# Performance work log

Measured on AMD Instinct MI355X. Metric: run time of the kernel, lower is better.

The kernel has to match this reference:

```python
import jax, jax.numpy as jnp
import numpy as np

EPS = 1e-5  # BatchNorm eps (torch default); BN is in training mode with gamma=1, beta=0 (init values)


def bn(x, axes):
    m = jnp.mean(x, axis=axes, keepdims=True)
    v = jnp.var(x, axis=axes, keepdims=True)
    return (x - m) * jax.lax.rsqrt(v + EPS)


def knn_idx(xyz, k):
    # brute-force squared-distance matrix [B,N,N], k smallest
    d = jnp.sum((xyz[:, :, None, :] - xyz[:, None, :, :]) ** 2, axis=-1)
    _, idx = jax.lax.top_k(-d, k)
    return idx  # [B,N,k]


def gather(x, idx):
    # x: [B,N,C], idx: [B,N,k] -> [B,N,k,C]
    return jax.vmap(lambda a, i: a[i])(x, idx)


def lse(xyz, features, idx, w):
    nbr_xyz = gather(xyz, idx)                       # [B,N,k,3]
    rel = nbr_xyz - xyz[:, :, None, :]
    dist = jnp.sqrt(jnp.maximum(jnp.sum(rel ** 2, -1, keepdims=True), 1e-12))
    nbr_f = gather(features, idx)                    # [B,N,k,C]
    enc = jnp.concatenate([rel, dist, nbr_f], -1)    # [B,N,k,C+4]
    return jax.nn.relu(bn(jnp.einsum('bnkc,oc->bnko', enc, w), (0, 1, 2)))


def att_pool(x, sw1, sw2, sb2, mw):
    # x: [B,N,k,C]
    h = jax.nn.relu(bn(jnp.einsum('bnkc,oc->bnko', x, sw1), (0, 1, 2)))
    scores = jax.nn.softmax(jnp.einsum('bnkc,oc->bnko', h, sw2) + sb2, axis=2)  # softmax over k
    feat = jnp.sum(x * scores, axis=2)               # [B,N,C]
    return jax.nn.relu(bn(jnp.einsum('bnc,oc->bno', feat, mw), (0, 1)))


def drb(x, w1, w2):
    # in_channels == out_channels -> identity shortcut
    h = jax.nn.relu(bn(jnp.einsum('bnc,oc->bno', x, w1), (0, 1)))
    h = bn(jnp.einsum('bnc,oc->bno', h, w2), (0, 1))
    return jax.nn.relu(h + x)


def setup_inputs() -> dict:
    key = jax.random.key(0)
    B, N, C, K, OUT = 4, 8192, 32, 16, 128
    H = OUT // 2  # 64
    ks = jax.random.split(key, 16)
    s = 0.05
    return {
        'xyz': jax.random.normal(ks[0], (B, N, 3), jnp.float32),
        'features': jax.random.normal(ks[1], (B, N, C), jnp.float32),
        'w_lse1': jax.random.normal(ks[2], (H, C + 4), jnp.float32) * s,
        'w_lse2': jax.random.normal(ks[3], (H, C + 4), jnp.float32) * s,
        'ap1_sw1': jax.random.normal(ks[4], (H, H), jnp.float32) * s,
        'ap1_sw2': jax.random.normal(ks[5], (1, H), jnp.float32) * s,
        'ap1_sb2': jax.random.normal(ks[6], (1,), jnp.float32) * s,
        'ap1_mw': jax.random.normal(ks[7], (H, H), jnp.float32) * s,
        'ap2_sw1': jax.random.normal(ks[8], (H, H), jnp.float32) * s,
        'ap2_sw2': jax.random.normal(ks[9], (1, H), jnp.float32) * s,
        'ap2_sb2': jax.random.normal(ks[10], (1,), jnp.float32) * s,
        'ap2_mw': jax.random.normal(ks[11], (H, H), jnp.float32) * s,
        'drb_w1': jax.random.normal(ks[12], (OUT, OUT), jnp.float32) * s,
        'drb_w2': jax.random.normal(ks[13], (OUT, OUT), jnp.float32) * s,
    }


def reference(xyz, features, w_lse1, w_lse2, ap1_sw1, ap1_sw2, ap1_sb2, ap1_mw,
              ap2_sw1, ap2_sw2, ap2_sb2, ap2_mw, drb_w1, drb_w2):
    K = 16
    idx = knn_idx(xyz, K)  # original calls knn twice on same xyz -> identical indices
    f1 = att_pool(lse(xyz, features, idx, w_lse1), ap1_sw1, ap1_sw2, ap1_sb2, ap1_mw)
    f2 = att_pool(lse(xyz, features, idx, w_lse2), ap2_sw1, ap2_sw2, ap2_sb2, ap2_mw)
    agg = jnp.concatenate([f1, f2], axis=-1)  # [B,N,128]
    return drb(agg, drb_w1, drb_w2)           # [B,N,128]
```

## Files before the change

### kernel.cpp

```cpp
#include <hip/hip_runtime.h>
#include <hip/hip_bf16.h>
#include <hip/hip_fp16.h>
#include <float.h>
#include <math.h>

#define DEVFN __device__ __forceinline__

DEVFN void wavefence() { __builtin_amdgcn_wave_barrier(); }

using half8 = __attribute__((ext_vector_type(8))) _Float16;
using f32x4 = __attribute__((ext_vector_type(4))) float;

namespace {
constexpr int Bq = 4, Nq = 8192, Cq = 32, Kq = 16;
constexpr int PTS = Bq * Nq;
constexpr int CH = 16;
constexpr int CAND = Nq / CH;
constexpr double ROWS = 524288.0;

constexpr int DS_Y = 0, DS_Z = 256, DS_G = 512, DS_H1 = 768, DS_H2 = 1024;

constexpr size_t OFF_KD   = 0;
constexpr size_t OFF_KJ   = (size_t)32 << 20;
constexpr size_t OFF_X0   = 0;
constexpr size_t OFF_X1   = (size_t)64 << 20;
constexpr size_t OFF_ENC  = (size_t)128 << 20;
constexpr size_t OFF_H1   = 0;
constexpr size_t OFF_H2   = (size_t)16 << 20;
constexpr size_t OFF_GRAW = (size_t)192 << 20;
constexpr size_t OFF_AGG  = (size_t)208 << 20;
constexpr size_t OFF_IDX  = (size_t)224 << 20;
constexpr size_t OFF_DST  = (size_t)226 << 20;
constexpr size_t OFF_MST  = ((size_t)226 << 20) + 10240;
constexpr size_t OFF_BNP  = ((size_t)226 << 20) + 16384;
constexpr size_t WS_NEED  = ((size_t)226 << 20) + 32768;
constexpr size_t FB_GRAW  = (size_t)64 << 20;
constexpr size_t FB_AGG   = (size_t)80 << 20;
constexpr size_t FB_H1    = (size_t)96 << 20;
constexpr size_t FB_H2    = (size_t)112 << 20;
constexpr size_t FB_IDX   = (size_t)128 << 20;
constexpr size_t FB_DST   = (size_t)130 << 20;
constexpr size_t FB_MST   = ((size_t)130 << 20) + 10240;
constexpr size_t FB_BNP   = ((size_t)130 << 20) + 16384;
}

DEVFN void ce_asc(float& a, float& b) {
  const float lo = fminf(a, b), hi = fmaxf(a, b);
  a = lo; b = hi;
}

DEVFN void topk16_update(float* __restrict__ L, float* __restrict__ d) {
#pragma unroll
  for (int k = 2; k <= 16; k <<= 1) {
#pragma unroll
    for (int j = k >> 1; j > 0; j >>= 1) {
#pragma unroll
      for (int i = 0; i < 16; ++i) {
        const int l = i ^ j;
        if (l > i) {
          if ((i & k) == 0) {
            const float lo = fminf(d[i], d[l]), hi = fmaxf(d[i], d[l]);
            d[i] = lo; d[l] = hi;
          } else {
            const float lo = fminf(d[i], d[l]), hi = fmaxf(d[i], d[l]);
            d[i] = hi; d[l] = lo;
          }
        }
      }
    }
  }
#pragma unroll
  for (int i = 0; i < 16; ++i) L[i] = fminf(L[i], d[15 - i]);
#pragma unroll
  for (int j = 8; j > 0; j >>= 1) {
#pragma unroll
    for (int i = 0; i < 16; ++i) {
      const int l = i ^ j;
      if (l > i) ce_asc(L[i], L[l]);
    }
  }
}

DEVFN float distf(const float4 c, const float qx, const float qy, const float qz) {
  const float dx = qx - c.x, dy = qy - c.y, dz = qz - c.z;
  return __fadd_rn(__fadd_rn(__fmul_rn(dx, dx), __fmul_rn(dy, dy)), __fmul_rn(dz, dz));
}

__global__ __launch_bounds__(256, 4) void knn_chunk_kernel(const float* __restrict__ xyz,
                                                           float* __restrict__ pd,
                                                           int* __restrict__ pj) {
  const int b = blockIdx.z;
  const int ch = blockIdx.y;
  const int n = blockIdx.x * 256 + threadIdx.x;
  __shared__ __align__(16) float4 tile[CAND];
  const float* xb = xyz + (size_t)b * Nq * 3;
  for (int t = threadIdx.x; t < CAND; t += 256) {
    const int j = ch * CAND + t;
    tile[t] = make_float4(xb[j * 3], xb[j * 3 + 1], xb[j * 3 + 2], 0.f);
  }
  __syncthreads();
  const float qx = xb[n * 3], qy = xb[n * 3 + 1], qz = xb[n * 3 + 2];
  float L[16];
#pragma unroll
  for (int i = 0; i < 16; ++i) L[i] = FLT_MAX;
  for (int t = 0; t < CAND; t += 16) {
    float d[16];
#pragma unroll
    for (int u = 0; u < 16; ++u) d[u] = distf(tile[t + u], qx, qy, qz);
// ... 110 lines not shown
    for (int q = 0; q < 4; ++q) {
      const __half2 xv = u.h[q];
      const __half2 wv = wh2[r * 4 + q];
      if (q & 1) {
        a2 += __low2float(xv) * __low2float(wv);
        a3 += __high2float(xv) * __high2float(wv);
      } else {
        a0 += __low2float(xv) * __low2float(wv);
        a1 += __high2float(xv) * __high2float(wv);
      }
    }
  }
  return (a0 + a1) + (a2 + a3);
}

DEVFN float dot64x(const __half* __restrict__ xr, const __half2* __restrict__ sh2) {
  float a0 = 0.f, a1 = 0.f, a2 = 0.f, a3 = 0.f;
#pragma unroll
  for (int r = 0; r < 8; ++r) {
    union { float4 f; __half2 h[4]; } u;
    u.f = *(const float4*)(xr + r * 8);
#pragma unroll
    for (int q = 0; q < 4; ++q) {
      const __half2 xv = u.h[q];
      const __half2 wv = sh2[r * 4 + q];
      if (q & 1) {
        a2 += __low2float(xv) * __low2float(wv);
        a3 += __high2float(xv) * __high2float(wv);
      } else {
        a0 += __low2float(xv) * __low2float(wv);
        a1 += __high2float(xv) * __high2float(wv);
      }
    }
  }
  return (a0 + a1) + (a2 + a3);
}

DEVFN void load_w40(const float* __restrict__ Wrow, __half2* wh2) {
#pragma unroll
  for (int c = 0; c < 16; ++c)
    wh2[c] = __floats2half2_rn(Wrow[4 + 2 * c], Wrow[5 + 2 * c]);
  wh2[16] = __floats2half2_rn(Wrow[0], Wrow[1]);
  wh2[17] = __floats2half2_rn(Wrow[2], Wrow[3]);
  wh2[18] = __floats2half2_rn(0.f, 0.f);
  wh2[19] = wh2[18];
}

DEVFN void load_b1(const float* __restrict__ W, int lane, half8* b1) {
  const int o16 = lane & 15, q = lane >> 4;
#pragma unroll
  for (int t = 0; t < 4; ++t) {
    const int o = t * 16 + o16;
#pragma unroll
    for (int ks = 0; ks < 2; ++ks) {
      half8 v;
#pragma unroll
      for (int j = 0; j < 8; ++j) {
        const int s = ks * 32 + q * 8 + j;
        float wv = 0.f;
        if (s < 36) { const int orig = (s < 32) ? (s + 4) : (s - 32); wv = W[o * 36 + orig]; }
        v[j] = (_Float16)wv;
      }
      b1[t * 2 + ks] = v;
    }
  }
}

DEVFN void load_b2(const float* __restrict__ S1, int lane, half8* b2) {
  const int o16 = lane & 15, q = lane >> 4;
#pragma unroll
  for (int t = 0; t < 4; ++t) {
    const int o = t * 16 + o16;
#pragma unroll
    for (int ks = 0; ks < 2; ++ks) {
      half8 v;
#pragma unroll
      for (int j = 0; j < 8; ++j) {
        const int c = ks * 32 + q * 8 + j;
        v[j] = (_Float16)S1[o * 64 + c];
      }
      b2[t * 2 + ks] = v;
    }
  }
}

#define GATHER_PROLOGUE                                                      \
  int p = wid;                                                               \
  int jc = issue_idx(idx, p, lane);                                          \
  PF cur = issue_feat(features, xyz, p, jc, lane & 3);                       \
  float3 qc = issue_query(xyz, p);                                           \
  int pn0 = p + nw; if (pn0 >= PTS) pn0 = p;                                 \
  int jn = issue_idx(idx, pn0, lane);                                        \
  float3 qn = issue_query(xyz, pn0);                                         \
  for (; p < PTS; p += nw) {                                                 \
    int pn = p + nw; if (pn >= PTS) pn = p;                                  \
    int pn2 = pn + nw; if (pn2 >= PTS) pn2 = pn;                             \
    PF nxt = issue_feat(features, xyz, pn, jn, lane & 3);                    \
    const int jn2 = issue_idx(idx, pn2, lane);                               \
    const float3 q2 = issue_query(xyz, pn2);                                 \
    commit_enc(enc, lane, cur, qc.x, qc.y, qc.z);                            \
    wavefence();

#define GATHER_EPILOGUE                                                      \
    wavefence();                                                             \
    cur = nxt; qc = qn; qn = q2; jn = jn2;                                   \
  }

__global__ __launch_bounds__(256)
void encM2_kernel(const float* __restrict__ xyz,
                  const float* __restrict__ features,
                  const int* __restrict__ idx,
                  const float* __restrict__ wl1,
                  const float* __restrict__ wl2,
                  double* __restrict__ dstat,
                  __half* __restrict__ encb) {
  __shared__ __align__(16) __half encS[4][16 * 40];
  const int lane = threadIdx.x & 63, wv = threadIdx.x >> 6;
  __half* enc = encS[wv];
  zero_enc_pad(enc, lane);
  wavefence();
  half8 b1a[8], b1b[8];
  load_b1(wl1, lane, b1a);
  load_b1(wl2, lane, b1b);
  const int r16 = lane & 15, q4 = lane >> 4;
  float ya1[4] = {0.f, 0.f, 0.f, 0.f}, ya2[4] = {0.f, 0.f, 0.f, 0.f};
  float yb1[4] = {0.f, 0.f, 0.f, 0.f}, yb2[4] = {0.f, 0.f, 0.f, 0.f};
  const int wid = blockIdx.x * 4 + wv, nw = gridDim.x * 4;
  GATHER_PROLOGUE
#pragma unroll
    for (int it = 0; it < 2; ++it) {
      const int c = it * 64 + lane;
      if (c < 80) {
        const float4 v = *(const float4*)((const char*)enc + c * 16);
        *(float4*)((char*)encb + (size_t)p * 1280 + c * 16) = v;
      }
    }
    const __half* er = enc + r16 * 40;
    const half8 a0 = *(const half8*)(er + q4 * 8);
    half8 a1;
#pragma unroll
    for (int j = 0; j < 8; ++j) a1[j] = (_Float16)0.f;
    if (q4 == 0) a1 = *(const half8*)(er + 32);
#pragma unroll
    for (int t = 0; t < 4; ++t) {
      f32x4 acc = {0.f, 0.f, 0.f, 0.f};
      acc = __builtin_amdgcn_mfma_f32_16x16x32_f16(a0, b1a[t * 2], acc, 0, 0, 0);
      acc = __builtin_amdgcn_mfma_f32_16x16x32_f16(a1, b1a[t * 2 + 1], acc, 0, 0, 0);
#pragma unroll
      for (int rr = 0; rr < 4; ++rr) { const float yv = acc[rr]; ya1[t] += yv; ya2[t] += yv * yv; }
      f32x4 acc2 = {0.f, 0.f, 0.f, 0.f};
      acc2 = __builtin_amdgcn_mfma_f32_16x16x32_f16(a0, b1b[t * 2], acc2, 0, 0, 0);
      acc2 = __builtin_amdgcn_mfma_f32_16x16x32_f16(a1, b1b[t * 2 + 1], acc2, 0, 0, 0);
#pragma unroll
      for (int rr = 0; rr < 4; ++rr) { const float yv = acc2[rr]; yb1[t] += yv; yb2[t] += yv * yv; }
    }
  GATHER_EPILOGUE
#pragma unroll
  for (int t = 0; t < 4; ++t) {
    ya1[t] += __shfl_xor(ya1[t], 16, 64);  ya1[t] += __shfl_xor(ya1[t], 32, 64);
    ya2[t] += __shfl_xor(ya2[t], 16, 64);  ya2[t] += __shfl_xor(ya2[t], 32, 64);
    yb1[t] += __shfl_xor(yb1[t], 16, 64);  yb1[t] += __shfl_xor(yb1[t], 32, 64);
    yb2[t] += __shfl_xor(yb2[t], 16, 64);  yb2[t] += __shfl_xor(yb2[t], 32, 64);
  }
  if (lane < 16) {
#pragma unroll
    for (int t = 0; t < 4; ++t) {
      atomicAdd(&dstat[DS_Y + t * 16 + lane], (double)ya1[t]);
      atomicAdd(&dstat[DS_Y + 128 + t * 16 + lane], (double)ya2[t]);
      atomicAdd(&dstat[DS_Y + 64 + t * 16 + lane], (double)yb1[t]);
      atomicAdd(&dstat[DS_Y + 128 + 64 + t * 16 + lane], (double)yb2[t]);
    }
  }
}

__global__ __launch_bounds__(256) void encM_kernel(const float* __restrict__ xyz,
                                                   const float* __restrict__ features,
                                                   const int* __restrict__ idx,
                                                   float* __restrict__ mstat) {
  __shared__ __align__(16) __half encS[4][16 * 40];
  __shared__ float mred[4][36 * 37];
  const int lane = threadIdx.x & 63, wv = threadIdx.x >> 6;
  __half* enc = encS[wv];
  zero_enc_pad(enc, lane);
  wavefence();
  const int li = (lane < 36) ? lane : 0;
  float macc[36];
#pragma unroll
  for (int i = 0; i < 36; ++i) macc[i] = 0.f;
  float vacc = 0.f;
  const int wid = blockIdx.x * 4 + wv, nw = gridDim.x * 4;
  GATHER_PROLOGUE
#pragma unroll
    for (int k = 0; k < 16; ++k) {
      const __half* er = enc + k * 40;
      const float ei = __half2float(er[li]);
      vacc += ei;
#pragma unroll
      for (int r = 0; r < 5; ++r) {
        union { float4 f; __half2 h[4]; } u;
        u.f = *(const float4*)(er + r * 8);
#pragma unroll
        for (int q = 0; q < 4; ++q) {
          const int s = r * 8 + 2 * q;
          if (s < 36)     macc[s]     += ei * __low2float(u.h[q]);
          if (s + 1 < 36) macc[s + 1] += ei * __high2float(u.h[q]);
        }
      }
    }
  GATHER_EPILOGUE
  if (lane < 36) {
#pragma unroll
    for (int j = 0; j < 36; ++j) mred[wv][lane * 37 + j] = macc[j];
    mred[wv][lane * 37 + 36] = vacc;
  }
  __syncthreads();
  for (int t = threadIdx.x; t < 36 * 37; t += 256) {
    const float s = mred[0][t] + mred[1][t] + mred[2][t] + mred[3][t];
    atomicAdd(&mstat[t], s);
  }
}

__global__ void y_finalize_kernel(const float* __restrict__ mstat,
                                  const float* __restrict__ wl1,
                                  const float* __restrict__ wl2,
                                  float* __restrict__ bnp) {
  const int t = threadIdx.x;
  const int br = t >> 6, o = t & 63;
  const float* W = br ? wl2 : wl1;
  double wrow[36];
  for (int s = 0; s < 36; ++s) {
    const int orig = (s < 32) ? (s + 4) : (s - 32);
    wrow[s] = (double)W[o * 36 + orig];
  }
  double mean = 0.0, ey2 = 0.0;
  for (int i = 0; i < 36; ++i) {
    mean += wrow[i] * (double)mstat[i * 37 + 36];
    double rowacc = 0.0;
    for (int j = 0; j < 36; ++j) rowacc += wrow[j] * (double)mstat[i * 37 + j];
    ey2 += wrow[i] * rowacc;
  }
  const double invR = 1.0 / ROWS;
  mean *= invR; ey2 *= invR;
  const double var = ey2 - mean * mean;
  bnp[DS_Y + br * 64 + o] = (float)mean;
  bnp[DS_Y + 128 + br * 64 + o] = (float)(1.0 / sqrt(var + 1e-5));
}

__global__ void bn_finalize_kernel(const double* __restrict__ dstat, float* __restrict__ bnp,
                                   int base, double invc) {
  const int t = threadIdx.x;
  const double m = dstat[base + t] * invc;
  const double v = dstat[base + 128 + t] * invc - m * m;
  bnp[base + t] = (float)m;
  bnp[base + 128 + t] = (float)(1.0 / sqrt(v + 1e-5));
}

__global__ __launch_bounds__(256)
void passA2s_kernel(const __half* __restrict__ encbuf,
                    const float* __restrict__ wl1,
                    const float* __restrict__ wl2,
                    const float* __restrict__ s1a,
                    const float* __restrict__ s1b,
                    const float* __restrict__ bnp,
                    double* __restrict__ dstat,
                    __half* __restrict__ x0buf,
                    __half* __restrict__ x1buf) {
  __shared__ __align__(16) __half xS[4][16 * 64];
  const int lane = threadIdx.x & 63, wv = threadIdx.x >> 6;
  __half* xL = xS[wv];
  half8 b1a[8], b1b[8], b2a[8], b2b[8];
  load_b1(wl1, lane, b1a);
  load_b1(wl2, lane, b1b);
  load_b2(s1a, lane, b2a);
  load_b2(s1b, lane, b2b);
  const int r16 = lane & 15, q4 = lane >> 4;
  float ym0[4], ys0[4], ym1[4], ys1[4];
#pragma unroll
  for (int t = 0; t < 4; ++t) {
    ym0[t] = bnp[DS_Y + t * 16 + r16];
    ys0[t] = bnp[DS_Y + 128 + t * 16 + r16];
    ym1[t] = bnp[DS_Y + 64 + t * 16 + r16];
    ys1[t] = bnp[DS_Y + 128 + 64 + t * 16 + r16];
  }
  float sa1[4] = {0.f, 0.f, 0.f, 0.f}, sa2[4] = {0.f, 0.f, 0.f, 0.f};
  float sb1[4] = {0.f, 0.f, 0.f, 0.f}, sb2s[4] = {0.f, 0.f, 0.f, 0.f};
  const int wid = blockIdx.x * 4 + wv, nw = gridDim.x * 4;
  for (int p = wid; p < PTS; p += nw) {
    const size_t eb = (size_t)p * 640 + r16 * 40 + q4 * 8;
    const half8 a0 = *(const half8*)(encbuf + eb);
    half8 a1;
#pragma unroll
    for (int j = 0; j < 8; ++j) a1[j] = (_Float16)0.f;
    if (q4 == 0) a1 = *(const half8*)(encbuf + eb + 32);
    {
      f32x4 yt[4];
#pragma unroll
      for (int t = 0; t < 4; ++t) {
        f32x4 acc = {0.f, 0.f, 0.f, 0.f};
        acc = __builtin_amdgcn_mfma_f32_16x16x32_f16(a0, b1a[t * 2], acc, 0, 0, 0);
        acc = __builtin_amdgcn_mfma_f32_16x16x32_f16(a1, b1a[t * 2 + 1], acc, 0, 0, 0);
        yt[t] = acc;
      }
#pragma unroll
      for (int t = 0; t < 4; ++t) {
        const int col = t * 16 + r16;
        const int chk = col >> 3;
#pragma unroll
        for (int rr = 0; rr < 4; ++rr) {
          const int row = q4 * 4 + rr;
          float xv = (yt[t][rr] - ym0[t]) * ys0[t];
          xv = xv > 0.f ? xv : 0.f;
          *(_Float16*)((char*)xL + row * 128 + ((chk ^ (row & 7)) * 16) + (col & 7) * 2) =
              (_Float16)xv;
        }
      }
      wavefence();
#pragma unroll
      for (int it = 0; it < 2; ++it) {
        const int chunk = it * 64 + lane;
        const int row = chunk >> 3, c8 = chunk & 7;
        const float4 xv4 = *(const float4*)((const char*)xL + row * 128 + ((c8 ^ (row & 7)) * 16));
        *(float4*)((char*)x0buf + (size_t)p * 2048 + chunk * 16) = xv4;
      }
      const char* xlb = (const char*)xL + r16 * 128;
      const half8 xa0 = *(const half8*)(xlb + (((q4)     ^ (r16 & 7)) * 16));
      const half8 xa1 = *(const half8*)(xlb + (((4 + q4) ^ (r16 & 7)) * 16));
#pragma unroll
      for (int t = 0; t < 4; ++t) {
        f32x4 acc = {0.f, 0.f, 0.f, 0.f};
        acc = __builtin_amdgcn_mfma_f32_16x16x32_f16(xa0, b2a[t * 2], acc, 0, 0, 0);
        acc = __builtin_amdgcn_mfma_f32_16x16x32_f16(xa1, b2a[t * 2 + 1], acc, 0, 0, 0);
#pragma unroll
        for (int rr = 0; rr < 4; ++rr) { const float zv = acc[rr]; sa1[t] += zv; sa2[t] += zv * zv; }
      }
      wavefence();
    }
    {
      f32x4 yt[4];
#pragma unroll
      for (int t = 0; t < 4; ++t) {
        f32x4 acc = {0.f, 0.f, 0.f, 0.f};
        acc = __builtin_amdgcn_mfma_f32_16x16x32_f16(a0, b1b[t * 2], acc, 0, 0, 0);
        acc = __builtin_amdgcn_mfma_f32_16x16x32_f16(a1, b1b[t * 2 + 1], acc, 0, 0, 0);
        yt[t] = acc;
      }
#pragma unroll
      for (int t = 0; t < 4; ++t) {
        const int col = t * 16 + r16;
        const int chk = col >> 3;
#pragma unroll
        for (int rr = 0; rr < 4; ++rr) {
          const int row = q4 * 4 + rr;
          float xv = (yt[t][rr] - ym1[t]) * ys1[t];
          xv = xv > 0.f ? xv : 0.f;
          *(_Float16*)((char*)xL + row * 128 + ((chk ^ (row & 7)) * 16) + (col & 7) * 2) =
              (_Float16)xv;
        }
      }
      wavefence();
#pragma unroll
      for (int it = 0; it < 2; ++it) {
        const int chunk = it * 64 + lane;
        const int row = chunk >> 3, c8 = chunk & 7;
        const float4 xv4 = *(const float4*)((const char*)xL + row * 128 + ((c8 ^ (row & 7)) * 16));
        *(float4*)((char*)x1buf + (size_t)p * 2048 + chunk * 16) = xv4;
      }
      const char* xlb = (const char*)xL + r16 * 128;
      const half8 xb0 = *(const half8*)(xlb + (((q4)     ^ (r16 & 7)) * 16));
      const half8 xb1 = *(const half8*)(xlb + (((4 + q4) ^ (r16 & 7)) * 16));
#pragma unroll
      for (int t = 0; t < 4; ++t) {
        f32x4 acc = {0.f, 0.f, 0.f, 0.f};
        acc = __builtin_amdgcn_mfma_f32_16x16x32_f16(xb0, b2b[t * 2], acc, 0, 0, 0);
        acc = __builtin_amdgcn_mfma_f32_16x16x32_f16(xb1, b2b[t * 2 + 1], acc, 0, 0, 0);
#pragma unroll
        for (int rr = 0; rr < 4; ++rr) { const float zv = acc[rr]; sb1[t] += zv; sb2s[t] += zv * zv; }
      }
      wavefence();
    }
  }
#pragma unroll
  for (int t = 0; t < 4; ++t) {
    sa1[t] += __shfl_xor(sa1[t], 16, 64);  sa1[t] += __shfl_xor(sa1[t], 32, 64);
    sa2[t] += __shfl_xor(sa2[t], 16, 64);  sa2[t] += __shfl_xor(sa2[t], 32, 64);
    sb1[t] += __shfl_xor(sb1[t], 16, 64);  sb1[t] += __shfl_xor(sb1[t], 32, 64);
    sb2s[t] += __shfl_xor(sb2s[t], 16, 64); sb2s[t] += __shfl_xor(sb2s[t], 32, 64);
  }
  if (lane < 16) {
#pragma unroll
    for (int t = 0; t < 4; ++t) {
      atomicAdd(&dstat[DS_Z + t * 16 + lane], (double)sa1[t]);
      atomicAdd(&dstat[DS_Z + 128 + t * 16 + lane], (double)sa2[t]);
      atomicAdd(&dstat[DS_Z + 64 + t * 16 + lane], (double)sb1[t]);
      atomicAdd(&dstat[DS_Z + 128 + 64 + t * 16 + lane], (double)sb2s[t]);
    }
  }
}

__global__ __launch_bounds__(256)
void passB2_mat_kernel(const __half* __restrict__ x0,
                       const __half* __restrict__ x1,
                       const float* __restrict__ s1a,
                       const float* __restrict__ s1b,
                       const float* __restrict__ s2a,
                       const float* __restrict__ s2b,
                       const float* __restrict__ sba,
                       const float* __restrict__ sbb,
                       const float* __restrict__ mwa,
                       const float* __restrict__ mwb,
                       const float* __restrict__ bnp,
                       double* __restrict__ dstat,
                       float* __restrict__ graw) {
  const int br = blockIdx.y;
  const __half* xbuf = br ? x1 : x0;
  const float* S1 = br ? s1b : s1a;
  const float* s2 = br ? s2b : s2a;
  const float* sb = br ? sbb : sba;
  const float* mw = br ? mwb : mwa;
  __shared__ __align__(16) __half2 mwl2[64 * 34];
  __shared__ __align__(16) float featL[4][64];
  __shared__ __align__(16) float zS[4][16 * 64];
  for (int t = threadIdx.x; t < 64 * 32; t += 256) {
    const int r = t >> 5, c2 = t & 31;
    mwl2[r * 34 + c2] = __floats2half2_rn(mw[r * 64 + c2 * 2], mw[r * 64 + c2 * 2 + 1]);
  }
  __syncthreads();
  const int lane = threadIdx.x & 63, wv = threadIdx.x >> 6;
  const int r16 = lane & 15, q4 = lane >> 4;
  half8 b2[8];
  load_b2(S1, lane, b2);
  const __half2* mrow = mwl2 + lane * 34;
  const float zm = bnp[DS_Z + br * 64 + lane];
  const float zsc = bnp[DS_Z + 128 + br * 64 + lane];
  const float sw2r = s2[lane];
  const float sb2v = sb[0];
  float gs1 = 0.f, gs2 = 0.f;
  float* zw = &zS[wv][0];
  const int wid = blockIdx.x * 4 + wv, nw = gridDim.x * 4;
  for (int p = wid; p < PTS; p += nw) {
    const size_t abase = (size_t)p * 1024 + r16 * 64 + q4 * 8;
    const half8 xa0 = *(const half8*)(xbuf + abase);
    const half8 xa1 = *(const half8*)(xbuf + abase + 32);
#pragma unroll
    for (int t = 0; t < 4; ++t) {
      f32x4 acc = {0.f, 0.f, 0.f, 0.f};
      acc = __builtin_amdgcn_mfma_f32_16x16x32_f16(xa0, b2[t * 2], acc, 0, 0, 0);
      acc = __builtin_amdgcn_mfma_f32_16x16x32_f16(xa1, b2[t * 2 + 1], acc, 0, 0, 0);
#pragma unroll
      for (int rr = 0; rr < 4; ++rr)
        zw[(q4 * 4 + rr) * 64 + t * 16 + r16] = acc[rr];
    }
    wavefence();
    const __half* xr = xbuf + (size_t)p * 1024 + lane;
    const float* zr = zw + lane;
    float xv[16], pl[16];
#pragma unroll
    for (int k = 0; k < 16; ++k) {
      xv[k] = __half2float(xr[k * 64]);
      float h = (zr[k * 64] - zm) * zsc;
      h = h > 0.f ? h : 0.f;
      pl[k] = h * sw2r;
    }
#pragma unroll
    for (int off = 1; off < 64; off <<= 1) {
#pragma unroll
      for (int k = 0; k < 16; ++k) pl[k] += __shfl_xor(pl[k], off, 64);
    }
    float mx = -FLT_MAX;
#pragma unroll
    for (int k = 0; k < 16; ++k) { pl[k] += sb2v; mx = fmaxf(mx, pl[k]); }
    float se = 0.f;
#pragma unroll
    for (int k = 0; k < 16; ++k) { pl[k] = expf(pl[k] - mx); se += pl[k]; }
    const float inv = 1.f / se;
    float f = 0.f;
#pragma unroll
    for (int k = 0; k < 16; ++k) f += xv[k] * (pl[k] * inv);
    featL[wv][lane] = f;
    wavefence();
    const float* featW = &featL[wv][0];
    float g0 = 0.f, g1 = 0.f, g2 = 0.f, g3 = 0.f;
#pragma unroll
    for (int c8 = 0; c8 < 8; ++c8) {
      const float4 fa = *(const float4*)(featW + c8 * 8);
      const float4 fb = *(const float4*)(featW + c8 * 8 + 4);
      const __half2 m0 = mrow[c8 * 4 + 0];
      const __half2 m1 = mrow[c8 * 4 + 1];
      const __half2 m2 = mrow[c8 * 4 + 2];
      const __half2 m3 = mrow[c8 * 4 + 3];
      g0 += fa.x * __low2float(m0); g1 += fa.y * __high2float(m0);
      g2 += fa.z * __low2float(m1); g3 += fa.w * __high2float(m1);
      g0 += fb.x * __low2float(m2); g1 += fb.y * __high2float(m2);
      g2 += fb.z * __low2float(m3); g3 += fb.w * __high2float(m3);
    }
    const float g = (g0 + g1) + (g2 + g3);
    graw[((size_t)br * PTS + p) * 64 + lane] = g;
    gs1 += g; gs2 += g * g;
    wavefence();
  }
  atomicAdd(&dstat[DS_G + br * 64 + lane], (double)gs1);
  atomicAdd(&dstat[DS_G + 128 + br * 64 + lane], (double)gs2);
}

__global__ __launch_bounds__(256)
void passA_kernel(const float* __restrict__ xyz,
                  const float* __restrict__ features,
                  const int* __restrict__ idx,
                  const float* __restrict__ wl1,
                  const float* __restrict__ wl2,
                  const float* __restrict__ s1a,
                  const float* __restrict__ s1b,
                  const float* __restrict__ bnp,
                  double* __restrict__ dstat) {
  const int br = blockIdx.y;
  const float* W = br ? wl2 : wl1;
  const float* S1 = br ? s1b : s1a;
  __shared__ __align__(16) __half encS[4][16 * 40];
  __shared__ __align__(16) __half xS[4][16 * 64];
  const int lane = threadIdx.x & 63, wv = threadIdx.x >> 6;
  __half* enc = encS[wv];
  __half* xL = xS[wv];
  zero_enc_pad(enc, lane);
  wavefence();
  __half2 wh2[20];
  load_w40(W + lane * 36, wh2);
  __half2 sh2[32];
#pragma unroll
  for (int c = 0; c < 32; ++c)
    sh2[c] = __floats2half2_rn(S1[lane * 64 + 2 * c], S1[lane * 64 + 2 * c + 1]);
  const float ym = bnp[DS_Y + br * 64 + lane];
  const float ys = bnp[DS_Y + 128 + br * 64 + lane];
  float zs1 = 0.f, zs2 = 0.f;
  const int wid = blockIdx.x * 4 + wv, nw = gridDim.x * 4;
  GATHER_PROLOGUE
#pragma unroll
    for (int k = 0; k < 16; ++k) {
      float xv = (dot40h(enc + k * 40, wh2) - ym) * ys;
      xv = xv > 0.f ? xv : 0.f;
      xL[k * 64 + lane] = __float2half(xv);
    }
    wavefence();
// ... 145 lines not shown
    rowS[wv][64 + lane] = v1;
    if (aggout) {
      aggout[(size_t)p * 128 + lane] = v0;
      aggout[(size_t)p * 128 + 64 + lane] = v1;
    }
    wavefence();
#pragma unroll
    for (int h = 0; h < 2; ++h) {
      const int o = h * 64 + lane;
      float b0 = 0.f, b1 = 0.f, b2 = 0.f, b3 = 0.f;
#pragma unroll
      for (int c4 = 0; c4 < 32; ++c4) {
        const float4 rv = *(const float4*)(&rowS[wv][c4 * 4]);
        b0 += rv.x * wlds[o * 129 + c4 * 4 + 0];
        b1 += rv.y * wlds[o * 129 + c4 * 4 + 1];
        b2 += rv.z * wlds[o * 129 + c4 * 4 + 2];
        b3 += rv.w * wlds[o * 129 + c4 * 4 + 3];
      }
      const float acc = (b0 + b1) + (b2 + b3);
      rowout[(size_t)p * 128 + o] = acc;
      if (h == 0) { a1s0 += acc; a2s0 += acc * acc; }
      else        { a1s1 += acc; a2s1 += acc * acc; }
    }
    wavefence();
  }
  atomicAdd(&dstat[dsOut + lane], (double)a1s0);
  atomicAdd(&dstat[dsOut + 64 + lane], (double)a1s1);
  atomicAdd(&dstat[dsOut + 128 + lane], (double)a2s0);
  atomicAdd(&dstat[dsOut + 128 + 64 + lane], (double)a2s1);
}

__global__ __launch_bounds__(256) void final_kernel(const float* __restrict__ h2,
                                                    const float* __restrict__ agg,
                                                    const float* __restrict__ bnp,
                                                    float* __restrict__ out) {
  const size_t e = (size_t)blockIdx.x * 256 + threadIdx.x;
  const int ch = (int)(e & 127);
  const float m = bnp[DS_H2 + ch], s = bnp[DS_H2 + 128 + ch];
  float v = (h2[e] - m) * s + agg[e];
  out[e] = v > 0.f ? v : 0.f;
}

extern "C" void kernel_launch(void* const* d_in, const int* in_sizes, int n_in,
                              void* d_out, int out_size, void* d_ws, size_t ws_size,
                              hipStream_t stream) {
  (void)in_sizes; (void)n_in; (void)out_size;
  const float* xyz      = (const float*)d_in[0];
  const float* features = (const float*)d_in[1];
  const float* w_lse1   = (const float*)d_in[2];
  const float* w_lse2   = (const float*)d_in[3];
  const float* ap1_sw1  = (const float*)d_in[4];
  const float* ap1_sw2  = (const float*)d_in[5];
  const float* ap1_sb2  = (const float*)d_in[6];
  const float* ap1_mw   = (const float*)d_in[7];
  const float* ap2_sw1  = (const float*)d_in[8];
  const float* ap2_sw2  = (const float*)d_in[9];
  const float* ap2_sb2  = (const float*)d_in[10];
  const float* ap2_mw   = (const float*)d_in[11];
  const float* drb_w1   = (const float*)d_in[12];
  const float* drb_w2   = (const float*)d_in[13];

  char* ws = (char*)d_ws;
  const bool mat = (ws_size >= WS_NEED);

  float*  knn_d = (float*)(ws + OFF_KD);
  int*    knn_j = (int*)(ws + OFF_KJ);
  int*    idx   = (int*)(ws + (mat ? OFF_IDX : FB_IDX));
  double* dstat = (double*)(ws + (mat ? OFF_DST : FB_DST));
  float*  mstat = (float*)(ws + (mat ? OFF_MST : FB_MST));
  float*  bnp   = (float*)(ws + (mat ? OFF_BNP : FB_BNP));
  float*  graw  = (float*)(ws + (mat ? OFF_GRAW : FB_GRAW));
  float*  agg   = (float*)(ws + (mat ? OFF_AGG : FB_AGG));
  float*  h1    = (float*)(ws + (mat ? OFF_H1 : FB_H1));
  float*  h2    = (float*)(ws + (mat ? OFF_H2 : FB_H2));
  float*  out   = (float*)d_out;

  (void)hipMemsetAsync(dstat, 0, 1280 * sizeof(double) + 36 * 37 * sizeof(float), stream);

  knn_chunk_kernel<<<dim3(Nq / 256, CH, Bq), 256, 0, stream>>>(xyz, knn_d, knn_j);
  knn_merge_kernel<<<dim3(PTS / 256), 256, 0, stream>>>(knn_d, knn_j, idx);

  if (mat) {
    __half* encb = (__half*)(ws + OFF_ENC);
    __half* x0 = (__half*)(ws + OFF_X0);
    __half* x1 = (__half*)(ws + OFF_X1);
    encM2_kernel<<<dim3(1280), 256, 0, stream>>>(xyz, features, idx, w_lse1, w_lse2,
                                                 dstat, encb);
    bn_finalize_kernel<<<1, 128, 0, stream>>>(dstat, bnp, DS_Y, 1.0 / ROWS);
    passA2s_kernel<<<dim3(1024), 256, 0, stream>>>(encb, w_lse1, w_lse2,
                                                   ap1_sw1, ap2_sw1, bnp, dstat, x0, x1);
    bn_finalize_kernel<<<1, 128, 0, stream>>>(dstat, bnp, DS_Z, 1.0 / ROWS);
    passB2_mat_kernel<<<dim3(1024, 2), 256, 0, stream>>>(x0, x1, ap1_sw1, ap2_sw1,
                                                         ap1_sw2, ap2_sw2, ap1_sb2, ap2_sb2,
                                                         ap1_mw, ap2_mw, bnp, dstat, graw);
  } else {
    encM_kernel<<<dim3(1280), 256, 0, stream>>>(xyz, features, idx, mstat);
    y_finalize_kernel<<<1, 128, 0, stream>>>(mstat, w_lse1, w_lse2, bnp);
    passA_kernel<<<dim3(640, 2), 256, 0, stream>>>(xyz, features, idx, w_lse1, w_lse2,
                                                   ap1_sw1, ap2_sw1, bnp, dstat);
    bn_finalize_kernel<<<1, 128, 0, stream>>>(dstat, bnp, DS_Z, 1.0 / ROWS);
    passB_kernel<<<dim3(512, 2), 256, 0, stream>>>(xyz, features, idx, w_lse1, w_lse2,
                                                   ap1_sw1, ap2_sw1, ap1_sw2, ap2_sw2,
                                                   ap1_sb2, ap2_sb2, ap1_mw, ap2_mw,
                                                   bnp, dstat, graw);
  }
  bn_finalize_kernel<<<1, 128, 0, stream>>>(dstat, bnp, DS_G, 1.0 / PTS);

  drb_mm_kernel<<<dim3(512), 256, 0, stream>>>(graw, drb_w1, bnp, dstat, agg, h1,
                                               DS_G, DS_H1, 0);
  bn_finalize_kernel<<<1, 128, 0, stream>>>(dstat, bnp, DS_H1, 1.0 / PTS);

  drb_mm_kernel<<<dim3(512), 256, 0, stream>>>(h1, drb_w2, bnp, dstat, nullptr, h2,
                                               DS_H1, DS_H2, 1);
  bn_finalize_kernel<<<1, 128, 0, stream>>>(dstat, bnp, DS_H2, 1.0 / PTS);

  final_kernel<<<dim3(PTS * 128 / 256), 256, 0, stream>>>(h2, agg, bnp, out);
}
```

Before: 1.185 ms.

## Recompute LSE activations in pass B instead of materializing x0/x1 buffers

```diff
diff --git a/kernel.cpp b/kernel.cpp
--- a/kernel.cpp
+++ b/kernel.cpp
@@ -22,8 +22,6 @@
 
 constexpr size_t OFF_KD   = 0;
 constexpr size_t OFF_KJ   = (size_t)32 << 20;
-constexpr size_t OFF_X0   = 0;
-constexpr size_t OFF_X1   = (size_t)64 << 20;
 constexpr size_t OFF_ENC  = (size_t)128 << 20;
 constexpr size_t OFF_H1   = 0;
 constexpr size_t OFF_H2   = (size_t)16 << 20;
@@ -300,6 +298,45 @@
       b2[t * 2 + ks] = v;
     }
   }
+}
+
+DEVFN void mfma_y(const half8 a0, const half8 a1, const half8* b1, f32x4* yt) {
+#pragma unroll
+  for (int t = 0; t < 4; ++t) {
+    f32x4 acc = {0.f, 0.f, 0.f, 0.f};
+    acc = __builtin_amdgcn_mfma_f32_16x16x32_f16(a0, b1[t * 2], acc, 0, 0, 0);
+    acc = __builtin_amdgcn_mfma_f32_16x16x32_f16(a1, b1[t * 2 + 1], acc, 0, 0, 0);
+    yt[t] = acc;
+  }
+}
+
+DEVFN void bn_relu_to_xl(__half* __restrict__ xL, const f32x4* yt,
+                         const float* ym, const float* ys, int r16, int q4) {
+#pragma unroll
+  for (int t = 0; t < 4; ++t) {
+    const int col = t * 16 + r16;
+    const int chk = col >> 3;
+#pragma unroll
+    for (int rr = 0; rr < 4; ++rr) {
+      const int row = q4 * 4 + rr;
+      float xv = (yt[t][rr] - ym[t]) * ys[t];
+      xv = xv > 0.f ? xv : 0.f;
+      *(_Float16*)((char*)xL + row * 128 + ((chk ^ (row & 7)) * 16) + (col & 7) * 2) =
+          (_Float16)xv;
+    }
+  }
+}
+
+DEVFN void xl_afrags(const __half* __restrict__ xL, int r16, int q4,
+                     half8& xa0, half8& xa1) {
+  const char* xlb = (const char*)xL + r16 * 128;
+  xa0 = *(const half8*)(xlb + (((q4)     ^ (r16 & 7)) * 16));
+  xa1 = *(const half8*)(xlb + (((4 + q4) ^ (r16 & 7)) * 16));
+}
+
+DEVFN float xl_elem(const __half* __restrict__ xL, int k, int lane) {
+  return __half2float(*(const __half*)((const char*)xL + k * 128 +
+                      ((((lane >> 3)) ^ (k & 7)) * 16) + (lane & 7) * 2));
 }
 
 #define GATHER_PROLOGUE                                                      \
@@ -359,19 +396,17 @@
 #pragma unroll
     for (int j = 0; j < 8; ++j) a1[j] = (_Float16)0.f;
     if (q4 == 0) a1 = *(const half8*)(er + 32);
-#pragma unroll
-    for (int t = 0; t < 4; ++t) {
-      f32x4 acc = {0.f, 0.f, 0.f, 0.f};
-      acc = __builtin_amdgcn_mfma_f32_16x16x32_f16(a0, b1a[t * 2], acc, 0, 0, 0);
-      acc = __builtin_amdgcn_mfma_f32_16x16x32_f16(a1, b1a[t * 2 + 1], acc, 0, 0, 0);
-#pragma unroll
-      for (int rr = 0; rr < 4; ++rr) { const float yv = acc[rr]; ya1[t] += yv; ya2[t] += yv * yv; }
-      f32x4 acc2 = {0.f, 0.f, 0.f, 0.f};
-      acc2 = __builtin_amdgcn_mfma_f32_16x16x32_f16(a0, b1b[t * 2], acc2, 0, 0, 0);
-      acc2 = __builtin_amdgcn_mfma_f32_16x16x32_f16(a1, b1b[t * 2 + 1], acc2, 0, 0, 0);
-#pragma unroll
-      for (int rr = 0; rr < 4; ++rr) { const float yv = acc2[rr]; yb1[t] += yv; yb2[t] += yv * yv; }
-    }
+    f32x4 yt[4];
+    mfma_y(a0, a1, b1a, yt);
+#pragma unroll
+    for (int t = 0; t < 4; ++t)
+#pragma unroll
+      for (int rr = 0; rr < 4; ++rr) { const float yv = yt[t][rr]; ya1[t] += yv; ya2[t] += yv * yv; }
+    mfma_y(a0, a1, b1b, yt);
+#pragma unroll
+    for (int t = 0; t < 4; ++t)
+#pragma unroll
+      for (int rr = 0; rr < 4; ++rr) { const float yv = yt[t][rr]; yb1[t] += yv; yb2[t] += yv * yv; }
   GATHER_EPILOGUE
 #pragma unroll
   for (int t = 0; t < 4; ++t) {
@@ -474,34 +509,30 @@
 }
 
 __global__ __launch_bounds__(256)
-void passA2s_kernel(const __half* __restrict__ encbuf,
+void zx_stat_kernel(const __half* __restrict__ encbuf,
                     const float* __restrict__ wl1,
                     const float* __restrict__ wl2,
                     const float* __restrict__ s1a,
                     const float* __restrict__ s1b,
                     const float* __restrict__ bnp,
-                    double* __restrict__ dstat,
-                    __half* __restrict__ x0buf,
-                    __half* __restrict__ x1buf) {
+                    double* __restrict__ dstat) {
+  const int br = blockIdx.y;
+  const float* W = br ? wl2 : wl1;
+  const float* S1 = br ? s1b : s1a;
   __shared__ __align__(16) __half xS[4][16 * 64];
   const int lane = threadIdx.x & 63, wv = threadIdx.x >> 6;
   __half* xL = xS[wv];
-  half8 b1a[8], b1b[8], b2a[8], b2b[8];
-  load_b1(wl1, lane, b1a);
-  load_b1(wl2, lane, b1b);
-  load_b2(s1a, lane, b2a);
-  load_b2(s1b, lane, b2b);
+  half8 b1[8], b2[8];
+  load_b1(W, lane, b1);
+  load_b2(S1, lane, b2);
   const int r16 = lane & 15, q4 = lane >> 4;
-  float ym0[4], ys0[4], ym1[4], ys1[4];
+  float ym[4], ys[4];
 #pragma unroll
   for (int t = 0; t < 4; ++t) {
-    ym0[t] = bnp[DS_Y + t * 16 + r16];
-    ys0[t] = bnp[DS_Y + 128 + t * 16 + r16];
-    ym1[t] = bnp[DS_Y + 64 + t * 16 + r16];
-    ys1[t] = bnp[DS_Y + 128 + 64 + t * 16 + r16];
-  }
-  float sa1[4] = {0.f, 0.f, 0.f, 0.f}, sa2[4] = {0.f, 0.f, 0.f, 0.f};
-  float sb1[4] = {0.f, 0.f, 0.f, 0.f}, sb2s[4] = {0.f, 0.f, 0.f, 0.f};
+    ym[t] = bnp[DS_Y + br * 64 + t * 16 + r16];
+    ys[t] = bnp[DS_Y + 128 + br * 64 + t * 16 + r16];
+  }
+  float s1v[4] = {0.f, 0.f, 0.f, 0.f}, s2v[4] = {0.f, 0.f, 0.f, 0.f};
   const int wid = blockIdx.x * 4 + wv, nw = gridDim.x * 4;
   for (int p = wid; p < PTS; p += nw) {
     const size_t eb = (size_t)p * 640 + r16 * 40 + q4 * 8;
@@ -510,133 +541,60 @@
 #pragma unroll
     for (int j = 0; j < 8; ++j) a1[j] = (_Float16)0.f;
     if (q4 == 0) a1 = *(const half8*)(encbuf + eb + 32);
-    {
-      f32x4 yt[4];
-#pragma unroll
-      for (int t = 0; t < 4; ++t) {
-        f32x4 acc = {0.f, 0.f, 0.f, 0.f};
-        acc = __builtin_amdgcn_mfma_f32_16x16x32_f16(a0, b1a[t * 2], acc, 0, 0, 0);
-        acc = __builtin_amdgcn_mfma_f32_16x16x32_f16(a1, b1a[t * 2 + 1], acc, 0, 0, 0);
-        yt[t] = acc;
-      }
-#pragma unroll
-      for (int t = 0; t < 4; ++t) {
-        const int col = t * 16 + r16;
-        const int chk = col >> 3;
-#pragma unroll
-        for (int rr = 0; rr < 4; ++rr) {
-          const int row = q4 * 4 + rr;
-          float xv = (yt[t][rr] - ym0[t]) * ys0[t];
-          xv = xv > 0.f ? xv : 0.f;
-          *(_Float16*)((char*)xL + row * 128 + ((chk ^ (row & 7)) * 16) + (col & 7) * 2) =
-              (_Float16)xv;
-        }
-      }
-      wavefence();
-#pragma unroll
-      for (int it = 0; it < 2; ++it) {
-        const int chunk = it * 64 + lane;
-        const int row = chunk >> 3, c8 = chunk & 7;
-        const float4 xv4 = *(const float4*)((const char*)xL + row * 128 + ((c8 ^ (row & 7)) * 16));
-        *(float4*)((char*)x0buf + (size_t)p * 2048 + chunk * 16) = xv4;
-      }
-      const char* xlb = (const char*)xL + r16 * 128;
-      const half8 xa0 = *(const half8*)(xlb + (((q4)     ^ (r16 & 7)) * 16));
-      const half8 xa1 = *(const half8*)(xlb + (((4 + q4) ^ (r16 & 7)) * 16));
-#pragma unroll
-      for (int t = 0; t < 4; ++t) {
-        f32x4 acc = {0.f, 0.f, 0.f, 0.f};
-        acc = __builtin_amdgcn_mfma_f32_16x16x32_f16(xa0, b2a[t * 2], acc, 0, 0, 0);
-        acc = __builtin_amdgcn_mfma_f32_16x16x32_f16(xa1, b2a[t * 2 + 1], acc, 0, 0, 0);
-#pragma unroll
-        for (int rr = 0; rr < 4; ++rr) { const float zv = acc[rr]; sa1[t] += zv; sa2[t] += zv * zv; }
-      }
-      wavefence();
-    }
-    {
-      f32x4 yt[4];
-#pragma unroll
-      for (int t = 0; t < 4; ++t) {
-        f32x4 acc = {0.f, 0.f, 0.f, 0.f};
-        acc = __builtin_amdgcn_mfma_f32_16x16x32_f16(a0, b1b[t * 2], acc, 0, 0, 0);
-        acc = __builtin_amdgcn_mfma_f32_16x16x32_f16(a1, b1b[t * 2 + 1], acc, 0, 0, 0);
-        yt[t] = acc;
-      }
-#pragma unroll
-      for (int t = 0; t < 4; ++t) {
-        const int col = t * 16 + r16;
-        const int chk = col >> 3;
-#pragma unroll
-        for (int rr = 0; rr < 4; ++rr) {
-          const int row = q4 * 4 + rr;
-          float xv = (yt[t][rr] - ym1[t]) * ys1[t];
-          xv = xv > 0.f ? xv : 0.f;
-          *(_Float16*)((char*)xL + row * 128 + ((chk ^ (row & 7)) * 16) + (col & 7) * 2) =
-              (_Float16)xv;
-        }
-      }
-      wavefence();
-#pragma unroll
-      for (int it = 0; it < 2; ++it) {
-        const int chunk = it * 64 + lane;
-        const int row = chunk >> 3, c8 = chunk & 7;
-        const float4 xv4 = *(const float4*)((const char*)xL + row * 128 + ((c8 ^ (row & 7)) * 16));
-        *(float4*)((char*)x1buf + (size_t)p * 2048 + chunk * 16) = xv4;
-      }
-      const char* xlb = (const char*)xL + r16 * 128;
-      const half8 xb0 = *(const half8*)(xlb + (((q4)     ^ (r16 & 7)) * 16));
-      const half8 xb1 = *(const half8*)(xlb + (((4 + q4) ^ (r16 & 7)) * 16));
-#pragma unroll
-      for (int t = 0; t < 4; ++t) {
-        f32x4 acc = {0.f, 0.f, 0.f, 0.f};
-        acc = __builtin_amdgcn_mfma_f32_16x16x32_f16(xb0, b2b[t * 2], acc, 0, 0, 0);
-        acc = __builtin_amdgcn_mfma_f32_16x16x32_f16(xb1, b2b[t * 2 + 1], acc, 0, 0, 0);
-#pragma unroll
-        for (int rr = 0; rr < 4; ++rr) { const float zv = acc[rr]; sb1[t] += zv; sb2s[t] += zv * zv; }
-      }
-      wavefence();
-    }
+    f32x4 yt[4];
+    mfma_y(a0, a1, b1, yt);
+    bn_relu_to_xl(xL, yt, ym, ys, r16, q4);
+    wavefence();
+    half8 xa0, xa1;
+    xl_afrags(xL, r16, q4, xa0, xa1);
+#pragma unroll
+    for (int t = 0; t < 4; ++t) {
+      f32x4 acc = {0.f, 0.f, 0.f, 0.f};
+      acc = __builtin_amdgcn_mfma_f32_16x16x32_f16(xa0, b2[t * 2], acc, 0, 0, 0);
+      acc = __builtin_amdgcn_mfma_f32_16x16x32_f16(xa1, b2[t * 2 + 1], acc, 0, 0, 0);
+#pragma unroll
+      for (int rr = 0; rr < 4; ++rr) { const float zv = acc[rr]; s1v[t] += zv; s2v[t] += zv * zv; }
+    }
+    wavefence();
   }
 #pragma unroll
   for (int t = 0; t < 4; ++t) {
-    sa1[t] += __shfl_xor(sa1[t], 16, 64);  sa1[t] += __shfl_xor(sa1[t], 32, 64);
-    sa2[t] += __shfl_xor(sa2[t], 16, 64);  sa2[t] += __shfl_xor(sa2[t], 32, 64);
-    sb1[t] += __shfl_xor(sb1[t], 16, 64);  sb1[t] += __shfl_xor(sb1[t], 32, 64);
-    sb2s[t] += __shfl_xor(sb2s[t], 16, 64); sb2s[t] += __shfl_xor(sb2s[t], 32, 64);
+    s1v[t] += __shfl_xor(s1v[t], 16, 64);  s1v[t] += __shfl_xor(s1v[t], 32, 64);
+    s2v[t] += __shfl_xor(s2v[t], 16, 64);  s2v[t] += __shfl_xor(s2v[t], 32, 64);
   }
   if (lane < 16) {
 #pragma unroll
     for (int t = 0; t < 4; ++t) {
-      atomicAdd(&dstat[DS_Z + t * 16 + lane], (double)sa1[t]);
-      atomicAdd(&dstat[DS_Z + 128 + t * 16 + lane], (double)sa2[t]);
-      atomicAdd(&dstat[DS_Z + 64 + t * 16 + lane], (double)sb1[t]);
-      atomicAdd(&dstat[DS_Z + 128 + 64 + t * 16 + lane], (double)sb2s[t]);
+      atomicAdd(&dstat[DS_Z + br * 64 + t * 16 + lane], (double)s1v[t]);
+      atomicAdd(&dstat[DS_Z + 128 + br * 64 + t * 16 + lane], (double)s2v[t]);
     }
   }
 }
 
 __global__ __launch_bounds__(256)
-void passB2_mat_kernel(const __half* __restrict__ x0,
-                       const __half* __restrict__ x1,
-                       const float* __restrict__ s1a,
-                       const float* __restrict__ s1b,
-                       const float* __restrict__ s2a,
-                       const float* __restrict__ s2b,
-                       const float* __restrict__ sba,
-                       const float* __restrict__ sbb,
-                       const float* __restrict__ mwa,
-                       const float* __restrict__ mwb,
-                       const float* __restrict__ bnp,
-                       double* __restrict__ dstat,
-                       float* __restrict__ graw) {
+void passB3_kernel(const __half* __restrict__ encbuf,
+                   const float* __restrict__ wl1,
+                   const float* __restrict__ wl2,
+                   const float* __restrict__ s1a,
+                   const float* __restrict__ s1b,
+                   const float* __restrict__ s2a,
+                   const float* __restrict__ s2b,
+                   const float* __restrict__ sba,
+                   const float* __restrict__ sbb,
+                   const float* __restrict__ mwa,
+                   const float* __restrict__ mwb,
+                   const float* __restrict__ bnp,
+                   double* __restrict__ dstat,
+                   float* __restrict__ graw) {
   const int br = blockIdx.y;
-  const __half* xbuf = br ? x1 : x0;
+  const float* W = br ? wl2 : wl1;
   const float* S1 = br ? s1b : s1a;
   const float* s2 = br ? s2b : s2a;
   const float* sb = br ? sbb : sba;
   const float* mw = br ? mwb : mwa;
   __shared__ __align__(16) __half2 mwl2[64 * 34];
   __shared__ __align__(16) float featL[4][64];
+  __shared__ __align__(16) __half xS[4][16 * 64];
   __shared__ __align__(16) float zS[4][16 * 64];
   for (int t = threadIdx.x; t < 64 * 32; t += 256) {
     const int r = t >> 5, c2 = t & 31;
@@ -645,20 +603,37 @@
   __syncthreads();
   const int lane = threadIdx.x & 63, wv = threadIdx.x >> 6;
   const int r16 = lane & 15, q4 = lane >> 4;
-  half8 b2[8];
+  __half* xL = xS[wv];
+  float* zw = &zS[wv][0];
+  half8 b1[8], b2[8];
+  load_b1(W, lane, b1);
   load_b2(S1, lane, b2);
   const __half2* mrow = mwl2 + lane * 34;
+  float ym[4], ys[4];
+#pragma unroll
+  for (int t = 0; t < 4; ++t) {
+    ym[t] = bnp[DS_Y + br * 64 + t * 16 + r16];
+    ys[t] = bnp[DS_Y + 128 + br * 64 + t * 16 + r16];
+  }
   const float zm = bnp[DS_Z + br * 64 + lane];
   const float zsc = bnp[DS_Z + 128 + br * 64 + lane];
   const float sw2r = s2[lane];
   const float sb2v = sb[0];
   float gs1 = 0.f, gs2 = 0.f;
-  float* zw = &zS[wv][0];
   const int wid = blockIdx.x * 4 + wv, nw = gridDim.x * 4;
   for (int p = wid; p < PTS; p += nw) {
-    const size_t abase = (size_t)p * 1024 + r16 * 64 + q4 * 8;
-    const half8 xa0 = *(const half8*)(xbuf + abase);
-    const half8 xa1 = *(const half8*)(xbuf + abase + 32);
+    const size_t eb = (size_t)p * 640 + r16 * 40 + q4 * 8;
+    const half8 a0 = *(const half8*)(encbuf + eb);
+    half8 a1;
+#pragma unroll
+    for (int j = 0; j < 8; ++j) a1[j] = (_Float16)0.f;
+    if (q4 == 0) a1 = *(const half8*)(encbuf + eb + 32);
+    f32x4 yt[4];
+    mfma_y(a0, a1, b1, yt);
+    bn_relu_to_xl(xL, yt, ym, ys, r16, q4);
+    wavefence();
+    half8 xa0, xa1;
+    xl_afrags(xL, r16, q4, xa0, xa1);
 #pragma unroll
     for (int t = 0; t < 4; ++t) {
       f32x4 acc = {0.f, 0.f, 0.f, 0.f};
@@ -669,12 +644,11 @@
         zw[(q4 * 4 + rr) * 64 + t * 16 + r16] = acc[rr];
     }
     wavefence();
-    const __half* xr = xbuf + (size_t)p * 1024 + lane;
     const float* zr = zw + lane;
     float xv[16], pl[16];
 #pragma unroll
     for (int k = 0; k < 16; ++k) {
-      xv[k] = __half2float(xr[k * 64]);
+      xv[k] = xl_elem(xL, k, lane);
       float h = (zr[k * 64] - zm) * zsc;
       h = h > 0.f ? h : 0.f;
       pl[k] = h * sw2r;
@@ -986,17 +960,15 @@
 
   if (mat) {
     __half* encb = (__half*)(ws + OFF_ENC);
-    __half* x0 = (__half*)(ws + OFF_X0);
-    __half* x1 = (__half*)(ws + OFF_X1);
     encM2_kernel<<<dim3(1280), 256, 0, stream>>>(xyz, features, idx, w_lse1, w_lse2,
                                                  dstat, encb);
     bn_finalize_kernel<<<1, 128, 0, stream>>>(dstat, bnp, DS_Y, 1.0 / ROWS);
-    passA2s_kernel<<<dim3(1024), 256, 0, stream>>>(encb, w_lse1, w_lse2,
-                                                   ap1_sw1, ap2_sw1, bnp, dstat, x0, x1);
+    zx_stat_kernel<<<dim3(1024, 2), 256, 0, stream>>>(encb, w_lse1, w_lse2,
+                                                      ap1_sw1, ap2_sw1, bnp, dstat);
     bn_finalize_kernel<<<1, 128, 0, stream>>>(dstat, bnp, DS_Z, 1.0 / ROWS);
-    passB2_mat_kernel<<<dim3(1024, 2), 256, 0, stream>>>(x0, x1, ap1_sw1, ap2_sw1,
-                                                         ap1_sw2, ap2_sw2, ap1_sb2, ap2_sb2,
-                                                         ap1_mw, ap2_mw, bnp, dstat, graw);
+    passB3_kernel<<<dim3(1024, 2), 256, 0, stream>>>(encb, w_lse1, w_lse2, ap1_sw1, ap2_sw1,
+                                                     ap1_sw2, ap2_sw2, ap1_sb2, ap2_sb2,
+                                                     ap1_mw, ap2_mw, bnp, dstat, graw);
   } else {
     encM_kernel<<<dim3(1280), 256, 0, stream>>>(xyz, features, idx, mstat);
     y_finalize_kernel<<<1, 128, 0, stream>>>(mstat, w_lse1, w_lse2, bnp);
```

New measurement: 1.234 ms. 4.1% more time.
